# Optimization experiments

Hardware: AMD Instinct MI355X
Metric: run time of the kernel (lower is better)

Reference implementation:

```python
import jax, jax.numpy as jnp
import numpy as np

B, N, DIM, H = 4, 16384, 384, 8
C = DIM // H          # head_dim = 48
M = C // 2            # kernel_ratio=0.5 -> m = 24
EPS = 1e-6

def setup_inputs() -> dict:
    key = jax.random.key(0)
    k0, k1, k2, k3, k4 = jax.random.split(key, 5)
    x = jax.random.normal(k0, (B, N, DIM), jnp.float32)
    # small init scale keeps exp() in the kernel feature map well-conditioned
    qkv_w = jax.random.normal(k1, (3 * DIM, DIM), jnp.float32) * 0.02
    proj_w = jax.random.normal(k2, (DIM, DIM), jnp.float32) * 0.02
    proj_b = jax.random.normal(k3, (DIM,), jnp.float32) * 0.02
    # per-head orthogonal random features (rows orthonormal), scaled by sqrt(m)
    g = jax.random.normal(k4, (H, C, M), jnp.float32)
    q_mat, _ = jnp.linalg.qr(g)                  # (H, C, M), orthonormal columns
    w = jnp.transpose(q_mat, (0, 2, 1)) * np.sqrt(M)  # (H, M, C)
    return {"x": x, "qkv_w": qkv_w, "proj_w": proj_w, "proj_b": proj_b, "w": w}

def _feature_map(t, w, scale):
    # t: [B,H,N,C], w: [H,M,C]
    t = t * scale
    logits = jnp.einsum('bhnc,hmc->bhnm', t, w) - 0.5 * jnp.sum(t * t, axis=-1, keepdims=True)
    return jnp.exp(logits) / np.sqrt(w.shape[1])

def reference(x, qkv_w, proj_w, proj_b, w):
    b, n, dim = x.shape
    h, m, c = w.shape
    scale = c ** (-0.25)
    # qkv projection, split into q,k,v with layout (qkv H C)
    qkv = (x @ qkv_w.T).reshape(b, n, 3, h, c).transpose(2, 0, 3, 1, 4)  # [3,B,H,N,C]
    q, k, v = qkv[0], qkv[1], qkv[2]
    phi_q = _feature_map(q, w, scale)   # [B,H,N,M]
    phi_k = _feature_map(k, w, scale)   # [B,H,N,M]
    # normalizer: q . sum_n(k)
    D = jnp.einsum('bhnm,bhm->bhn', phi_q, phi_k.sum(axis=2)) + EPS  # [B,H,N]
    # linear-attention state: K^T V, then Q @ (K^T V)
    ktv = jnp.einsum('bhnm,bhnc->bhmc', phi_k, v)                    # [B,H,M,C]
    out = jnp.einsum('bhnm,bhmc->bhnc', phi_q, ktv) / D[..., None]   # [B,H,N,C]
    out = out.transpose(0, 2, 1, 3).reshape(b, n, dim)               # [B,N,dim]
    return out @ proj_w.T + proj_b
```

## Files before the change

kernel.cpp:

```cpp
#include <hip/hip_runtime.h>
#include <hip/hip_bf16.h>

typedef __bf16 bf16x8 __attribute__((ext_vector_type(8)));
typedef float  f32x4  __attribute__((ext_vector_type(4)));
typedef short  short8 __attribute__((ext_vector_type(8)));
typedef float  f32x4v __attribute__((ext_vector_type(4)));

#define B_SZ 4
#define N_SZ 16384
#define DIM_SZ 384
#define H_SZ 8
#define C_SZ 48
#define M_SZ 24

static constexpr float SCALE = 0.37991784282579627f;
static constexpr float RSM   = 0.20412414523193154f;
static constexpr float EPS_V = 1e-6f;


__device__ __forceinline__ void gld_lds16(void* lds, const void* g) {
  __builtin_amdgcn_global_load_lds(
      (const __attribute__((address_space(1))) unsigned int*)g,
      (__attribute__((address_space(3))) unsigned int*)lds, 16, 0, 0);
}

__device__ __forceinline__ float bf2f(short s) {
  union { unsigned u; float f; } cv;
  cv.u = ((unsigned)(unsigned short)s) << 16;
  return cv.f;
}
__device__ __forceinline__ short f2bf_s(float f) {
  const __bf16 b = (__bf16)f;
  return __builtin_bit_cast(short, b);
}
__device__ __forceinline__ f32x4 MF(bf16x8 a, bf16x8 b, f32x4 c) {
  return __builtin_amdgcn_mfma_f32_16x16x32_bf16(a, b, c, 0, 0, 0);
}

template<int EPI>
__global__ __launch_bounds__(256, 2) void gemm2b(
    const __bf16* __restrict__ A, const __bf16* __restrict__ Bm,
    void* __restrict__ Cout, const float* __restrict__ bias,
    int M, int Nw, int K,
    size_t aSlice, size_t bSlice, size_t cSlice) {
  extern __shared__ __align__(16) char lds[];
  const int t    = threadIdx.x;
  const int lane = t & 63;
  const int wid  = t >> 6;
  const int wm   = wid >> 1;
  const int wn   = wid & 1;
  const int l15  = lane & 15;
  const int kgq  = lane >> 4;

  const int bz = blockIdx.z;
  const __bf16* Ab = A  + (size_t)bz * aSlice;
  const __bf16* Bb = Bm + (size_t)bz * bSlice;

  const int gx   = gridDim.x;
  const int nwg  = gx * gridDim.y;
  const int orig = blockIdx.y * gx + blockIdx.x;
  const int qq   = nwg >> 3, rr = nwg & 7;
  const int xcd  = orig & 7, pos = orig >> 3;
  const int id   = (xcd < rr ? xcd*(qq+1) : rr*(qq+1) + (xcd-rr)*qq) + pos;
  const int row0 = (id / gx) * 128, col0 = (id % gx) * 128;

  const int nt = K >> 6;
  const int sg = (t & 7) ^ ((t >> 3) & 7);

  auto stage = [&](int kt) {
    char* buf = lds + (kt & 1) * 32768;
    const size_t kofs = (size_t)kt * 64 + sg * 8;
    #pragma unroll
    for (int i = 0; i < 4; ++i) {
      const int r = i*32 + (t >> 3);
      gld_lds16(buf + i*4096 + t*16,         Ab + (size_t)(row0 + r) * K + kofs);
      gld_lds16(buf + 16384 + i*4096 + t*16, Bb + (size_t)(col0 + r) * K + kofs);
    }
  };

  f32x4 acc[4][4] = {};
  stage(0);

  for (int kt = 0; kt < nt; ++kt) {
    asm volatile("s_waitcnt vmcnt(0)" ::: "memory");
    __builtin_amdgcn_s_barrier();
    __builtin_amdgcn_sched_barrier(0);

    char* buf = lds + (kt & 1) * 32768;
    if (kt + 1 < nt) stage(kt + 1);

    bf16x8 bfr[4][2];
    #pragma unroll
    for (int ni = 0; ni < 4; ++ni) {
      const int brow = wn*64 + ni*16 + l15;
      #pragma unroll
      for (int kk = 0; kk < 2; ++kk)
        bfr[ni][kk] = *(const bf16x8*)(buf + 16384 + brow*128
                          + ((kk*64 + kgq*16) ^ ((brow & 7) << 4)));
    }
    #pragma unroll
    for (int mi = 0; mi < 4; ++mi) {
      const int arow = wm*64 + mi*16 + l15;
      const bf16x8 a0 = *(const bf16x8*)(buf + arow*128
                          + ((kgq*16)      ^ ((arow & 7) << 4)));
      const bf16x8 a1 = *(const bf16x8*)(buf + arow*128
                          + ((64 + kgq*16) ^ ((arow & 7) << 4)));
      __builtin_amdgcn_s_setprio(1);
      #pragma unroll
      for (int ni = 0; ni < 4; ++ni) {
        acc[mi][ni] = MF(a0, bfr[ni][0], acc[mi][ni]);
        acc[mi][ni] = MF(a1, bfr[ni][1], acc[mi][ni]);
      }
      __builtin_amdgcn_s_setprio(0);
    }
  }

  const int cr = (lane >> 4) << 2;
  #pragma unroll
  for (int mi = 0; mi < 4; ++mi) {
    #pragma unroll
    for (int ni = 0; ni < 4; ++ni) {
      const int col = col0 + wn*64 + ni*16 + l15;
      #pragma unroll
      for (int j = 0; j < 4; ++j) {
        const int row = row0 + wm*64 + mi*16 + cr + j;
        const float v = acc[mi][ni][j];
        if (EPI == 1) {
          ((float*)Cout + (size_t)bz*cSlice)[(size_t)row * Nw + col] = v + bias[col];
        } else {
          ((__bf16*)Cout + (size_t)bz*cSlice)[(size_t)row * Nw + col] = (__bf16)v;
        }
      }
    }
  }
}

__global__ __launch_bounds__(256) void wlog_kernel(
    const float* __restrict__ qkv_w, const float* __restrict__ w,
    __bf16* __restrict__ Baug) {
  const int idx = blockIdx.x * 256 + threadIdx.x;
  if (idx >= 2*192*384) return;
  const int d = idx % 384, rs = idx / 384;
  const int side = rs / 192, hm = rs % 192;
  const int h = hm / 24;
  const float* wr = w + (size_t)hm * 48;
  const float* qw = qkv_w + ((size_t)(side*384 + h*48)) * 384 + d;
  float acc = 0.f;
  #pragma unroll
  for (int c = 0; c < 48; ++c)
    acc += wr[c] * qw[(size_t)c * 384];
  Baug[(size_t)(768 + side*192 + hm) * 384 + d] = (__bf16)(acc * SCALE);
}

__global__ __launch_bounds__(256) void ktv_fused(
    const __bf16* __restrict__ kvll, float* __restrict__ ktv_part) {
  const int b = blockIdx.z, h = blockIdx.y, sp = blockIdx.x;
  const int t = threadIdx.x, wv = t >> 6, lane = t & 63;
  const int l15 = lane & 15, g = lane >> 4;
  const int bh = b*H_SZ + h;
  __shared__ __align__(16) __bf16 vT[4][48][40];
  __shared__ __align__(16) __bf16 phiT[4][24][40];
  __shared__ float red[4][1184];
  f32x4 acc[2][3] = {};
  f32x4 aks[2] = {};
  const int nbase = sp*256 + wv*64;

  bf16x8 ones{};
  if (l15 == 0)
    #pragma unroll
    for (int j = 0; j < 8; ++j) ones[j] = (__bf16)1.0f;

  for (int step = 0; step < 2; ++step) {
    const int n0 = nbase + step*32;
    #pragma unroll
    for (int it = 0; it < 3; ++it) {
      const int task = it*64 + lane;
      const int tk = task / 6, p = task % 6;
      const short8 r = *(const short8*)(kvll + ((size_t)(b*N_SZ) + n0 + tk)*1152
                                            + 384 + h*C_SZ + p*8);
      #pragma unroll
      for (int e = 0; e < 8; ++e)
        vT[wv][p*8 + e][tk] = __builtin_bit_cast(__bf16, (short)r[e]);
    }
    if (lane < 32) {
      const __bf16* row = kvll + ((size_t)(b*N_SZ) + n0 + lane)*1152 + h*C_SZ;
      float ss = 0.f;
      #pragma unroll
      for (int i = 0; i < 6; ++i) {
        const short8 r = *(const short8*)(row + i*8);
        #pragma unroll
        for (int j = 0; j < 8; ++j) { const float f = bf2f(r[j]) * SCALE; ss += f*f; }
      }
      const float hs = 0.5f * ss;
      const __bf16* lk = kvll + ((size_t)(b*N_SZ) + n0 + lane)*1152 + 960 + h*24;
      #pragma unroll
      for (int i = 0; i < 3; ++i) {
        const short8 r = *(const short8*)(lk + i*8);
        #pragma unroll
        for (int j = 0; j < 8; ++j)
          phiT[wv][i*8 + j][lane] = (__bf16)(__expf(bf2f(r[j]) - hs) * RSM);
      }
    }
    const bf16x8 a0 = *(const bf16x8*)(&phiT[wv][l15][g*8]);
    bf16x8 a1{};
    if (l15 < 8) a1 = *(const bf16x8*)(&phiT[wv][16 + l15][g*8]);
    #pragma unroll
    for (int ct = 0; ct < 3; ++ct) {
      const bf16x8 bfr = *(const bf16x8*)(&vT[wv][ct*16 + l15][g*8]);
      acc[0][ct] = MF(a0, bfr, acc[0][ct]);
      acc[1][ct] = MF(a1, bfr, acc[1][ct]);
    }
    aks[0] = MF(a0, ones, aks[0]);
    aks[1] = MF(a1, ones, aks[1]);
  }

  #pragma unroll
  for (int mt = 0; mt < 2; ++mt)
    #pragma unroll
    for (int ct = 0; ct < 3; ++ct)
      #pragma unroll
      for (int jj = 0; jj < 4; ++jj) {
        const int row = mt*16 + g*4 + jj;
        if (row < 24)
          red[wv][row*48 + ct*16 + l15] = acc[mt][ct][jj];
      }
  if (l15 == 0) {
    #pragma unroll
    for (int mt = 0; mt < 2; ++mt)
      #pragma unroll
      for (int jj = 0; jj < 4; ++jj) {
        const int m = mt*16 + g*4 + jj;
        if (m < 24) red[wv][1152 + m] = aks[mt][jj];
      }
  }
  __syncthreads();
  float* outp = ktv_part + ((size_t)bh*64 + sp) * 1184;
  for (int i = t; i < 1176; i += 256)
    outp[i] = red[0][i] + red[1][i] + red[2][i] + red[3][i];
}

__global__ __launch_bounds__(256) void reduce_ktv(
    const float* __restrict__ ktv_part, float* __restrict__ ktv_f,
    float* __restrict__ ksum) {
  const int bh = blockIdx.x >> 2, q = blockIdx.x & 3;
  const int i0 = q * 296;
  const int iend = (i0 + 296 < 1176) ? i0 + 296 : 1176;
  for (int i = i0 + threadIdx.x; i < iend; i += 256) {
    float s = 0.f;
    #pragma unroll 8
    for (int sp = 0; sp < 64; ++sp)
      s += ktv_part[((size_t)bh*64 + sp) * 1184 + i];
    if (i < 1152) ktv_f[bh*1152 + i] = s;
    else          ksum[bh*24 + (i - 1152)] = s;
  }
}

__global__ __launch_bounds__(256) void gt_kernel(
    const float* __restrict__ ktv_f, const float* __restrict__ proj_w,
    __bf16* __restrict__ Gt) {
  const int idx = blockIdx.x * 256 + threadIdx.x;
  if (idx >= 4*384*192) return;
  const int hm = idx % 192, o = (idx / 192) % 384, b = idx / (192*384);
  const int h = hm / 24, m = hm % 24;
  const float* kt = ktv_f + ((size_t)(b*H_SZ + h))*1152 + m*48;
  const float* pw = proj_w + (size_t)o*384 + h*48;
  float acc = 0.f;
  #pragma unroll
  for (int c = 0; c < 48; ++c) acc += kt[c] * pw[c];
  Gt[((size_t)b*384 + o)*192 + hm] = (__bf16)acc;
}

__global__ __launch_bounds__(256) void pprime_kernel(
    const __bf16* __restrict__ kvll, const float* __restrict__ ksum,
    __bf16* __restrict__ Pp) {
  const int tok = blockIdx.x * 256 + threadIdx.x;
  const int b = (blockIdx.x * 256) >> 14;
  __shared__ float ksl[192];
  if (threadIdx.x < 192) ksl[threadIdx.x] = ksum[b*192 + threadIdx.x];
  __syncthreads();

  const __bf16* lq = kvll + (size_t)tok*1152 + 768;
  __bf16* po = Pp + (size_t)tok*192;
  #pragma unroll
  for (int h = 0; h < 8; ++h) {
    float ph[24];
    float d = EPS_V;
    #pragma unroll
    for (int i = 0; i < 3; ++i) {
      const short8 r = *(const short8*)(lq + h*24 + i*8);
      #pragma unroll
      for (int j = 0; j < 8; ++j) {
        const float p = __expf(bf2f(r[j])) * RSM;
        ph[i*8 + j] = p;
        d += p * ksl[h*24 + i*8 + j];
      }
    }
    const float inv = 1.0f / d;
    #pragma unroll
    for (int i = 0; i < 3; ++i) {
      short8 pk;
      #pragma unroll
      for (int j = 0; j < 8; ++j) pk[j] = f2bf_s(ph[i*8 + j] * inv);
      *(short8*)(po + h*24 + i*8) = pk;
    }
  }
}

__global__ __launch_bounds__(256) void f32_to_bf16_kernel(
    const float* __restrict__ in, __bf16* __restrict__ out, int n8) {
  const int i = blockIdx.x * blockDim.x + threadIdx.x;
  if (i >= n8) return;
  const f32x4v a = *(const f32x4v*)(in + (size_t)i*8);
  const f32x4v c = *(const f32x4v*)(in + (size_t)i*8 + 4);
  short8 pk;
  #pragma unroll
  for (int j = 0; j < 4; ++j) {
    pk[j]     = f2bf_s(a[j]);
    pk[4 + j] = f2bf_s(c[j]);
  }
  *(short8*)(out + (size_t)i*8) = pk;
}

extern "C" void kernel_launch(void* const* d_in, const int* in_sizes, int n_in,
                              void* d_out, int out_size, void* d_ws, size_t ws_size,
                              hipStream_t stream) {
  (void)in_sizes; (void)n_in; (void)out_size; (void)ws_size;
  const float* x      = (const float*)d_in[0];
  const float* qkv_w  = (const float*)d_in[1];
  const float* proj_w = (const float*)d_in[2];
  const float* proj_b = (const float*)d_in[3];
  const float* w      = (const float*)d_in[4];
  float* out = (float*)d_out;

  const size_t BN_TOT = (size_t)B_SZ * N_SZ;
  char* ws = (char*)d_ws;
  size_t off = 0;
  auto alloc = [&](size_t bytes) {
    char* p = ws + off;
    off += (bytes + 255) & ~(size_t)255;
    return p;
  };
  __bf16* x_bf     = (__bf16*)alloc(BN_TOT * DIM_SZ * 2);
  __bf16* Baug     = (__bf16*)alloc((size_t)1152 * 384 * 2);
  __bf16* kvll     = (__bf16*)alloc(BN_TOT * 1152 * 2);
  float*  ktv_part = (float*)alloc((size_t)32 * 64 * 1184 * 4);
  float*  ktv_f    = (float*)alloc((size_t)32 * 1152 * 4);
  float*  ksum     = (float*)alloc((size_t)32 * 24 * 4);
  __bf16* Pp       = (__bf16*)alloc(BN_TOT * 192 * 2);
  __bf16* Gt       = (__bf16*)alloc((size_t)B_SZ * 384 * 192 * 2);

  static const int LDS2B = 2 * 32768;
  hipFuncSetAttribute(reinterpret_cast<const void*>(&gemm2b<0>),
                      hipFuncAttributeMaxDynamicSharedMemorySize, LDS2B);
  hipFuncSetAttribute(reinterpret_cast<const void*>(&gemm2b<1>),
                      hipFuncAttributeMaxDynamicSharedMemorySize, LDS2B);

  {
    const int n8x = (int)(BN_TOT * DIM_SZ / 8);
    f32_to_bf16_kernel<<<(n8x + 255)/256, 256, 0, stream>>>(x, x_bf, n8x);
    const int n8kv = 768 * 384 / 8;
    f32_to_bf16_kernel<<<(n8kv + 255)/256, 256, 0, stream>>>(
        qkv_w + (size_t)384 * 384, Baug, n8kv);
    wlog_kernel<<<(2*192*384 + 255)/256, 256, 0, stream>>>(qkv_w, w, Baug);
  }

  gemm2b<0><<<dim3(1152/128, BN_TOT/128, 1), 256, LDS2B, stream>>>(
      x_bf, Baug, kvll, nullptr, (int)BN_TOT, 1152, DIM_SZ, 0, 0, 0);

  ktv_fused<<<dim3(64, H_SZ, B_SZ), 256, 0, stream>>>(kvll, ktv_part);
  reduce_ktv<<<128, 256, 0, stream>>>(ktv_part, ktv_f, ksum);

  gt_kernel<<<(4*384*192 + 255)/256, 256, 0, stream>>>(ktv_f, proj_w, Gt);
  pprime_kernel<<<(int)(BN_TOT/256), 256, 0, stream>>>(kvll, ksum, Pp);

  gemm2b<1><<<dim3(384/128, N_SZ/128, B_SZ), 256, LDS2B, stream>>>(
      Pp, Gt, out, proj_b, N_SZ, 384, 192,
      (size_t)N_SZ * 192, (size_t)384 * 192, (size_t)N_SZ * 384);
}
```

Baseline: 196.6 us.

## Switch GEMM to triple-buffered K=32 tiles with deeper prefetch and 3 blocks/CU

The GEMM main loop changes from double-buffered 64-wide K tiles to triple-buffered 32-wide K tiles, prefetching two stages ahead and waiting only on the older stage's loads (vmcnt(4)). LDS per block drops from 64KB to 48KB and launch bounds rise to 3 blocks per CU, with a new 4-way XOR swizzle for the 64-byte rows. The aim is to hide global-to-LDS latency better and raise occupancy. In exchange there are twice as many barriers per K, fewer MFMAs per barrier, and tighter register limits.

```diff
diff --git a/kernel.cpp b/kernel.cpp
--- a/kernel.cpp
+++ b/kernel.cpp
@@ -38,7 +38,7 @@
 }
 
 template<int EPI>
-__global__ __launch_bounds__(256, 2) void gemm2b(
+__global__ __launch_bounds__(256, 3) void gemm3b(
     const __bf16* __restrict__ A, const __bf16* __restrict__ Bm,
     void* __restrict__ Cout, const float* __restrict__ bias,
     int M, int Nw, int K,
@@ -64,55 +64,54 @@
   const int id   = (xcd < rr ? xcd*(qq+1) : rr*(qq+1) + (xcd-rr)*qq) + pos;
   const int row0 = (id / gx) * 128, col0 = (id % gx) * 128;
 
-  const int nt = K >> 6;
-  const int sg = (t & 7) ^ ((t >> 3) & 7);
+  const int nt = K >> 5;
+
+  const int sg8 = ((t & 3) ^ ((t >> 2) & 3) ^ ((t >> 4) & 3)) * 8;
 
   auto stage = [&](int kt) {
-    char* buf = lds + (kt & 1) * 32768;
-    const size_t kofs = (size_t)kt * 64 + sg * 8;
-    #pragma unroll
-    for (int i = 0; i < 4; ++i) {
-      const int r = i*32 + (t >> 3);
-      gld_lds16(buf + i*4096 + t*16,         Ab + (size_t)(row0 + r) * K + kofs);
-      gld_lds16(buf + 16384 + i*4096 + t*16, Bb + (size_t)(col0 + r) * K + kofs);
+    char* buf = lds + (kt % 3) * 16384;
+    const size_t kofs = (size_t)kt * 32 + sg8;
+    #pragma unroll
+    for (int i = 0; i < 2; ++i) {
+      const int r = i*64 + (t >> 2);
+      gld_lds16(buf + i*4096 + t*16,        Ab + (size_t)(row0 + r) * K + kofs);
+      gld_lds16(buf + 8192 + i*4096 + t*16, Bb + (size_t)(col0 + r) * K + kofs);
     }
   };
 
   f32x4 acc[4][4] = {};
   stage(0);
+  if (nt > 1) stage(1);
 
   for (int kt = 0; kt < nt; ++kt) {
-    asm volatile("s_waitcnt vmcnt(0)" ::: "memory");
+    if (kt < nt - 1) asm volatile("s_waitcnt vmcnt(4)" ::: "memory");
+    else             asm volatile("s_waitcnt vmcnt(0)" ::: "memory");
     __builtin_amdgcn_s_barrier();
     __builtin_amdgcn_sched_barrier(0);
 
-    char* buf = lds + (kt & 1) * 32768;
-    if (kt + 1 < nt) stage(kt + 1);
-
-    bf16x8 bfr[4][2];
+    char* buf = lds + (kt % 3) * 16384;
+    if (kt + 2 < nt) stage(kt + 2);
+
+    bf16x8 af[4], bfr[4];
+    #pragma unroll
+    for (int mi = 0; mi < 4; ++mi) {
+      const int a = wm*64 + mi*16 + l15;
+      af[mi] = *(const bf16x8*)(buf + a*64
+                  + ((kgq*16) ^ ((((a & 3) ^ ((a >> 2) & 3))) << 4)));
+    }
     #pragma unroll
     for (int ni = 0; ni < 4; ++ni) {
-      const int brow = wn*64 + ni*16 + l15;
-      #pragma unroll
-      for (int kk = 0; kk < 2; ++kk)
-        bfr[ni][kk] = *(const bf16x8*)(buf + 16384 + brow*128
-                          + ((kk*64 + kgq*16) ^ ((brow & 7) << 4)));
-    }
-    #pragma unroll
-    for (int mi = 0; mi < 4; ++mi) {
-      const int arow = wm*64 + mi*16 + l15;
-      const bf16x8 a0 = *(const bf16x8*)(buf + arow*128
-                          + ((kgq*16)      ^ ((arow & 7) << 4)));
-      const bf16x8 a1 = *(const bf16x8*)(buf + arow*128
-                          + ((64 + kgq*16) ^ ((arow & 7) << 4)));
-      __builtin_amdgcn_s_setprio(1);
-      #pragma unroll
-      for (int ni = 0; ni < 4; ++ni) {
-        acc[mi][ni] = MF(a0, bfr[ni][0], acc[mi][ni]);
-        acc[mi][ni] = MF(a1, bfr[ni][1], acc[mi][ni]);
-      }
-      __builtin_amdgcn_s_setprio(0);
-    }
+      const int b = wn*64 + ni*16 + l15;
+      bfr[ni] = *(const bf16x8*)(buf + 8192 + b*64
+                  + ((kgq*16) ^ ((((b & 3) ^ ((b >> 2) & 3))) << 4)));
+    }
+    __builtin_amdgcn_s_setprio(1);
+    #pragma unroll
+    for (int mi = 0; mi < 4; ++mi)
+      #pragma unroll
+      for (int ni = 0; ni < 4; ++ni)
+        acc[mi][ni] = MF(af[mi], bfr[ni], acc[mi][ni]);
+    __builtin_amdgcn_s_setprio(0);
   }
 
   const int cr = (lane >> 4) << 2;
@@ -349,11 +348,11 @@
   __bf16* Pp       = (__bf16*)alloc(BN_TOT * 192 * 2);
   __bf16* Gt       = (__bf16*)alloc((size_t)B_SZ * 384 * 192 * 2);
 
-  static const int LDS2B = 2 * 32768;
-  hipFuncSetAttribute(reinterpret_cast<const void*>(&gemm2b<0>),
-                      hipFuncAttributeMaxDynamicSharedMemorySize, LDS2B);
-  hipFuncSetAttribute(reinterpret_cast<const void*>(&gemm2b<1>),
-                      hipFuncAttributeMaxDynamicSharedMemorySize, LDS2B);
+  static const int LDS3B = 3 * 16384;
+  hipFuncSetAttribute(reinterpret_cast<const void*>(&gemm3b<0>),
+                      hipFuncAttributeMaxDynamicSharedMemorySize, LDS3B);
+  hipFuncSetAttribute(reinterpret_cast<const void*>(&gemm3b<1>),
+                      hipFuncAttributeMaxDynamicSharedMemorySize, LDS3B);
 
   {
     const int n8x = (int)(BN_TOT * DIM_SZ / 8);
@@ -364,7 +363,7 @@
     wlog_kernel<<<(2*192*384 + 255)/256, 256, 0, stream>>>(qkv_w, w, Baug);
   }
 
-  gemm2b<0><<<dim3(1152/128, BN_TOT/128, 1), 256, LDS2B, stream>>>(
+  gemm3b<0><<<dim3(1152/128, BN_TOT/128, 1), 256, LDS3B, stream>>>(
       x_bf, Baug, kvll, nullptr, (int)BN_TOT, 1152, DIM_SZ, 0, 0, 0);
 
   ktv_fused<<<dim3(64, H_SZ, B_SZ), 256, 0, stream>>>(kvll, ktv_part);
@@ -373,7 +372,7 @@
   gt_kernel<<<(4*384*192 + 255)/256, 256, 0, stream>>>(ktv_f, proj_w, Gt);
   pprime_kernel<<<(int)(BN_TOT/256), 256, 0, stream>>>(kvll, ksum, Pp);
 
-  gemm2b<1><<<dim3(384/128, N_SZ/128, B_SZ), 256, LDS2B, stream>>>(
+  gemm3b<1><<<dim3(384/128, N_SZ/128, B_SZ), 256, LDS3B, stream>>>(
       Pp, Gt, out, proj_b, N_SZ, 384, 192,
       (size_t)N_SZ * 192, (size_t)384 * 192, (size_t)N_SZ * 384);
 }
```

Result: slower. 207.9 us (+5.8%).

## Merge prep and gt/pprime launches; stage ktv inputs through LDS with coalesced loads

Applied to the files above, without the earlier changes.

Three small prep kernels (x cast, qkv weight cast, feature-weight fold) become one launch that picks its branch by block index. The Gt and P' kernels are likewise merged into one launch. In ktv_fused, k and the k-logit slices are first loaded cooperatively into shared memory with coalesced 16-byte loads instead of per-lane strided row reads. The LDS buffers are unioned with the reduction buffer, which needs a __syncthreads before reuse. The aim is to cut launch overhead and improve memory coalescing, at the cost of branchy kernels with mixed work per block.

```diff
diff --git a/kernel.cpp b/kernel.cpp
--- a/kernel.cpp
+++ b/kernel.cpp
@@ -135,21 +135,47 @@
   }
 }
 
-__global__ __launch_bounds__(256) void wlog_kernel(
-    const float* __restrict__ qkv_w, const float* __restrict__ w,
+__global__ __launch_bounds__(256) void prep_kernel(
+    const float* __restrict__ x, const float* __restrict__ qkv_w,
+    const float* __restrict__ w, __bf16* __restrict__ x_bf,
     __bf16* __restrict__ Baug) {
-  const int idx = blockIdx.x * 256 + threadIdx.x;
-  if (idx >= 2*192*384) return;
-  const int d = idx % 384, rs = idx / 384;
-  const int side = rs / 192, hm = rs % 192;
-  const int h = hm / 24;
-  const float* wr = w + (size_t)hm * 48;
-  const float* qw = qkv_w + ((size_t)(side*384 + h*48)) * 384 + d;
-  float acc = 0.f;
-  #pragma unroll
-  for (int c = 0; c < 48; ++c)
-    acc += wr[c] * qw[(size_t)c * 384];
-  Baug[(size_t)(768 + side*192 + hm) * 384 + d] = (__bf16)(acc * SCALE);
+  const int bid = blockIdx.x, t = threadIdx.x;
+  if (bid < 12288) {
+    const int i = bid * 256 + t;
+    const f32x4v a = *(const f32x4v*)(x + (size_t)i*8);
+    const f32x4v c = *(const f32x4v*)(x + (size_t)i*8 + 4);
+    short8 pk;
+    #pragma unroll
+    for (int j = 0; j < 4; ++j) {
+      pk[j]     = f2bf_s(a[j]);
+      pk[4 + j] = f2bf_s(c[j]);
+    }
+    *(short8*)(x_bf + (size_t)i*8) = pk;
+  } else if (bid < 12432) {
+    const int i = (bid - 12288) * 256 + t;
+    const float* src = qkv_w + (size_t)384 * 384;
+    const f32x4v a = *(const f32x4v*)(src + (size_t)i*8);
+    const f32x4v c = *(const f32x4v*)(src + (size_t)i*8 + 4);
+    short8 pk;
+    #pragma unroll
+    for (int j = 0; j < 4; ++j) {
+      pk[j]     = f2bf_s(a[j]);
+      pk[4 + j] = f2bf_s(c[j]);
+    }
+    *(short8*)(Baug + (size_t)i*8) = pk;
+  } else {
+    const int idx = (bid - 12432) * 256 + t;
+    const int d = idx % 384, rs = idx / 384;
+    const int side = rs / 192, hm = rs % 192;
+    const int h = hm / 24;
+    const float* wr = w + (size_t)hm * 48;
+    const float* qw = qkv_w + ((size_t)(side*384 + h*48)) * 384 + d;
+    float acc = 0.f;
+    #pragma unroll
+    for (int c = 0; c < 48; ++c)
+      acc += wr[c] * qw[(size_t)c * 384];
+    Baug[(size_t)(768 + side*192 + hm) * 384 + d] = (__bf16)(acc * SCALE);
+  }
 }
 
 __global__ __launch_bounds__(256) void ktv_fused(
@@ -158,9 +184,14 @@
   const int t = threadIdx.x, wv = t >> 6, lane = t & 63;
   const int l15 = lane & 15, g = lane >> 4;
   const int bh = b*H_SZ + h;
-  __shared__ __align__(16) __bf16 vT[4][48][40];
-  __shared__ __align__(16) __bf16 phiT[4][24][40];
-  __shared__ float red[4][1184];
+
+  __shared__ __align__(16) char smem[47616];
+  __bf16 (*vT)[48][40]  = (__bf16(*)[48][40])(smem);
+  __bf16 (*phiT)[24][40]= (__bf16(*)[24][40])(smem + 15360);
+  __bf16 (*kS)[32][56]  = (__bf16(*)[32][56])(smem + 23040);
+  __bf16 (*lkS)[32][40] = (__bf16(*)[32][40])(smem + 37376);
+  float  (*red)[1184]   = (float(*)[1184])(smem);
+
   f32x4 acc[2][3] = {};
   f32x4 aks[2] = {};
   const int nbase = sp*256 + wv*64;
@@ -172,30 +203,49 @@
 
   for (int step = 0; step < 2; ++step) {
     const int n0 = nbase + step*32;
+    const __bf16* base = kvll + ((size_t)(b*N_SZ) + n0) * 1152;
     #pragma unroll
     for (int it = 0; it < 3; ++it) {
       const int task = it*64 + lane;
       const int tk = task / 6, p = task % 6;
-      const short8 r = *(const short8*)(kvll + ((size_t)(b*N_SZ) + n0 + tk)*1152
-                                            + 384 + h*C_SZ + p*8);
+      const short8 r = *(const short8*)(base + (size_t)tk*1152 + 384 + h*C_SZ + p*8);
       #pragma unroll
       for (int e = 0; e < 8; ++e)
         vT[wv][p*8 + e][tk] = __builtin_bit_cast(__bf16, (short)r[e]);
     }
+    #pragma unroll
+    for (int it = 0; it < 3; ++it) {
+      const int task = it*64 + lane;
+      const int tk = task / 6, p = task % 6;
+      const short8 r = *(const short8*)(base + (size_t)tk*1152 + h*C_SZ + p*8);
+      *(short8*)(&kS[wv][tk][p*8]) = r;
+    }
+    {
+      const int task0 = lane;
+      {
+        const int tk = task0 / 3, p = task0 % 3;
+        const short8 r = *(const short8*)(base + (size_t)tk*1152 + 960 + h*24 + p*8);
+        *(short8*)(&lkS[wv][tk][p*8]) = r;
+      }
+      if (lane < 32) {
+        const int task = 64 + lane;
+        const int tk = task / 3, p = task % 3;
+        const short8 r = *(const short8*)(base + (size_t)tk*1152 + 960 + h*24 + p*8);
+        *(short8*)(&lkS[wv][tk][p*8]) = r;
+      }
+    }
     if (lane < 32) {
-      const __bf16* row = kvll + ((size_t)(b*N_SZ) + n0 + lane)*1152 + h*C_SZ;
       float ss = 0.f;
       #pragma unroll
       for (int i = 0; i < 6; ++i) {
-        const short8 r = *(const short8*)(row + i*8);
+        const short8 r = *(const short8*)(&kS[wv][lane][i*8]);
         #pragma unroll
         for (int j = 0; j < 8; ++j) { const float f = bf2f(r[j]) * SCALE; ss += f*f; }
       }
       const float hs = 0.5f * ss;
-      const __bf16* lk = kvll + ((size_t)(b*N_SZ) + n0 + lane)*1152 + 960 + h*24;
       #pragma unroll
       for (int i = 0; i < 3; ++i) {
-        const short8 r = *(const short8*)(lk + i*8);
+        const short8 r = *(const short8*)(&lkS[wv][lane][i*8]);
         #pragma unroll
         for (int j = 0; j < 8; ++j)
           phiT[wv][i*8 + j][lane] = (__bf16)(__expf(bf2f(r[j]) - hs) * RSM);
@@ -213,6 +263,8 @@
     aks[0] = MF(a0, ones, aks[0]);
     aks[1] = MF(a1, ones, aks[1]);
   }
+
+  __syncthreads();
 
   #pragma unroll
   for (int mt = 0; mt < 2; ++mt)
@@ -255,28 +307,28 @@
   }
 }
 
-__global__ __launch_bounds__(256) void gt_kernel(
+__global__ __launch_bounds__(256) void gtpp_kernel(
     const float* __restrict__ ktv_f, const float* __restrict__ proj_w,
-    __bf16* __restrict__ Gt) {
-  const int idx = blockIdx.x * 256 + threadIdx.x;
-  if (idx >= 4*384*192) return;
-  const int hm = idx % 192, o = (idx / 192) % 384, b = idx / (192*384);
-  const int h = hm / 24, m = hm % 24;
-  const float* kt = ktv_f + ((size_t)(b*H_SZ + h))*1152 + m*48;
-  const float* pw = proj_w + (size_t)o*384 + h*48;
-  float acc = 0.f;
-  #pragma unroll
-  for (int c = 0; c < 48; ++c) acc += kt[c] * pw[c];
-  Gt[((size_t)b*384 + o)*192 + hm] = (__bf16)acc;
-}
-
-__global__ __launch_bounds__(256) void pprime_kernel(
     const __bf16* __restrict__ kvll, const float* __restrict__ ksum,
-    __bf16* __restrict__ Pp) {
-  const int tok = blockIdx.x * 256 + threadIdx.x;
-  const int b = (blockIdx.x * 256) >> 14;
+    __bf16* __restrict__ Gt, __bf16* __restrict__ Pp) {
+  const int bid = blockIdx.x, t = threadIdx.x;
+  if (bid < 1152) {
+    const int idx = bid * 256 + t;
+    const int hm = idx % 192, o = (idx / 192) % 384, b = idx / (192*384);
+    const int h = hm / 24, m = hm % 24;
+    const float* kt = ktv_f + ((size_t)(b*H_SZ + h))*1152 + m*48;
+    const float* pw = proj_w + (size_t)o*384 + h*48;
+    float acc = 0.f;
+    #pragma unroll
+    for (int c = 0; c < 48; ++c) acc += kt[c] * pw[c];
+    Gt[((size_t)b*384 + o)*192 + hm] = (__bf16)acc;
+    return;
+  }
+  const int blk = bid - 1152;
+  const int tok = blk * 256 + t;
+  const int b = (blk * 256) >> 14;
   __shared__ float ksl[192];
-  if (threadIdx.x < 192) ksl[threadIdx.x] = ksum[b*192 + threadIdx.x];
+  if (t < 192) ksl[t] = ksum[b*192 + t];
   __syncthreads();
 
   const __bf16* lq = kvll + (size_t)tok*1152 + 768;
@@ -304,21 +356,6 @@
       *(short8*)(po + h*24 + i*8) = pk;
     }
   }
-}
-
-__global__ __launch_bounds__(256) void f32_to_bf16_kernel(
-    const float* __restrict__ in, __bf16* __restrict__ out, int n8) {
-  const int i = blockIdx.x * blockDim.x + threadIdx.x;
-  if (i >= n8) return;
-  const f32x4v a = *(const f32x4v*)(in + (size_t)i*8);
-  const f32x4v c = *(const f32x4v*)(in + (size_t)i*8 + 4);
-  short8 pk;
-  #pragma unroll
-  for (int j = 0; j < 4; ++j) {
-    pk[j]     = f2bf_s(a[j]);
-    pk[4 + j] = f2bf_s(c[j]);
-  }
-  *(short8*)(out + (size_t)i*8) = pk;
 }
 
 extern "C" void kernel_launch(void* const* d_in, const int* in_sizes, int n_in,
@@ -355,14 +392,7 @@
   hipFuncSetAttribute(reinterpret_cast<const void*>(&gemm2b<1>),
                       hipFuncAttributeMaxDynamicSharedMemorySize, LDS2B);
 
-  {
-    const int n8x = (int)(BN_TOT * DIM_SZ / 8);
-    f32_to_bf16_kernel<<<(n8x + 255)/256, 256, 0, stream>>>(x, x_bf, n8x);
-    const int n8kv = 768 * 384 / 8;
-    f32_to_bf16_kernel<<<(n8kv + 255)/256, 256, 0, stream>>>(
-        qkv_w + (size_t)384 * 384, Baug, n8kv);
-    wlog_kernel<<<(2*192*384 + 255)/256, 256, 0, stream>>>(qkv_w, w, Baug);
-  }
+  prep_kernel<<<13008, 256, 0, stream>>>(x, qkv_w, w, x_bf, Baug);
 
   gemm2b<0><<<dim3(1152/128, BN_TOT/128, 1), 256, LDS2B, stream>>>(
       x_bf, Baug, kvll, nullptr, (int)BN_TOT, 1152, DIM_SZ, 0, 0, 0);
@@ -370,8 +400,7 @@
   ktv_fused<<<dim3(64, H_SZ, B_SZ), 256, 0, stream>>>(kvll, ktv_part);
   reduce_ktv<<<128, 256, 0, stream>>>(ktv_part, ktv_f, ksum);
 
-  gt_kernel<<<(4*384*192 + 255)/256, 256, 0, stream>>>(ktv_f, proj_w, Gt);
-  pprime_kernel<<<(int)(BN_TOT/256), 256, 0, stream>>>(kvll, ksum, Pp);
+  gtpp_kernel<<<1408, 256, 0, stream>>>(ktv_f, proj_w, kvll, ksum, Gt, Pp);
 
   gemm2b<1><<<dim3(384/128, N_SZ/128, B_SZ), 256, LDS2B, stream>>>(
       Pp, Gt, out, proj_b, N_SZ, 384, 192,
```

Measured after the change: 189.4 us. 1.04x faster.
